# Optimization experiments

Measured on AMD Instinct MI355X. Metric: run time of the kernel, lower is better.

The kernel has to match this reference:

```python
import jax, jax.numpy as jnp
import numpy as np


def setup_inputs() -> dict:
    key = jax.random.key(0)
    ks = jax.random.split(key, 5)
    B, D, U = 16384, 512, 512
    return {
        "inputs": jax.random.normal(ks[0], (B, D), dtype=jnp.float32),
        "h_prev": jax.random.normal(ks[1], (B, U), dtype=jnp.float32),
        "update_kernel": jax.random.normal(ks[2], (D + U, U), dtype=jnp.float32) * 0.03,
        "reset_kernel": jax.random.normal(ks[3], (D + U, U), dtype=jnp.float32) * 0.03,
        "hidden_kernel": jax.random.normal(ks[4], (D + U, U), dtype=jnp.float32) * 0.03,
        "update_bias": jnp.zeros((U,), dtype=jnp.float32),
        "reset_bias": jnp.zeros((U,), dtype=jnp.float32),
        "hidden_bias": jnp.zeros((U,), dtype=jnp.float32),
    }


def reference(inputs, h_prev, update_kernel, reset_kernel, hidden_kernel,
              update_bias, reset_bias, hidden_bias):
    # fused_input: [B, D+U]
    fused = jnp.concatenate([inputs, h_prev], axis=-1)
    zg = jax.nn.sigmoid(fused @ update_kernel + update_bias)   # update gate [B,U]
    rg = jax.nn.sigmoid(fused @ reset_kernel + reset_bias)     # reset gate  [B,U]
    h_tilde = jnp.tanh(
        jnp.concatenate([inputs, rg * h_prev], axis=-1) @ hidden_kernel + hidden_bias
    )
    ht = (1.0 - zg) * h_prev + zg * h_tilde
    return ht
```

## Files before the change

### kernel.cpp

```cpp
#include <hip/hip_runtime.h>
#include <hip/hip_bf16.h>
#include <math.h>

typedef __attribute__((ext_vector_type(4))) float f32x4;
typedef __attribute__((ext_vector_type(8))) float f32x8;
typedef __bf16 bf16x8 __attribute__((ext_vector_type(8)));
typedef unsigned short u16;
typedef u16 u16x8 __attribute__((ext_vector_type(8)));
typedef void __attribute__((address_space(1))) * as1p;
typedef void __attribute__((address_space(3))) * as3p;

__device__ __forceinline__ unsigned short f2bf(float f) {
    union { float f; unsigned int u; } v; v.f = f;
    unsigned int u = v.u;
    u += 0x7fffu + ((u >> 16) & 1u);
    return (unsigned short)(u >> 16);
}

__device__ __forceinline__ float bf2f(unsigned short b) {
    union { unsigned int u; float f; } v;
    v.u = ((unsigned int)b) << 16;
    return v.f;
}

__device__ __forceinline__ float fast_tanh(float v) {
    float vc = fminf(fmaxf(v, -15.f), 15.f);
    float e = __expf(2.f * vc);
    return (e - 1.f) / (e + 1.f);
}

__global__ void prep_k(const float* __restrict__ x, const float* __restrict__ h,
                       const float* __restrict__ wz, const float* __restrict__ wrr,
                       const float* __restrict__ wh,
                       u16* __restrict__ xb, u16* __restrict__ hb,
                       u16* __restrict__ wzt, u16* __restrict__ wrt, u16* __restrict__ wht) {
    __shared__ float t[32][33];
    int bid = blockIdx.x;
    int tid = threadIdx.x;
    if (bid < 2048) {
        const int n4 = 16384 * 512 / 4;
        int i = bid * 256 + tid;
        const int stride = 2048 * 256;
        const float4* x4 = (const float4*)x;
        const float4* h4 = (const float4*)h;
        ushort4* xb4 = (ushort4*)xb;
        ushort4* hb4 = (ushort4*)hb;
        for (; i < n4; i += stride) {
            float4 v = x4[i];
            xb4[i] = make_ushort4(f2bf(v.x), f2bf(v.y), f2bf(v.z), f2bf(v.w));
            float4 w = h4[i];
            hb4[i] = make_ushort4(f2bf(w.x), f2bf(w.y), f2bf(w.z), f2bf(w.w));
        }
    } else {
        int b = bid - 2048;
        int z = b >> 9;
        int rem = b & 511;
        const float* src = (z == 0) ? wz : (z == 1) ? wrr : wh;
        u16* dst = (z == 0) ? wzt : (z == 1) ? wrt : wht;
        int n0 = (rem & 15) * 32;
        int k0 = (rem >> 4) * 32;
        int tx = tid & 31, ty = tid >> 5;
#pragma unroll
        for (int i = 0; i < 4; ++i)
            t[ty + i * 8][tx] = src[(size_t)(k0 + ty + i * 8) * 512 + n0 + tx];
        __syncthreads();
#pragma unroll
        for (int i = 0; i < 4; ++i)
            dst[(size_t)(n0 + ty + i * 8) * 1024 + k0 + tx] = f2bf(t[tx][ty + i * 8]);
    }
}

__device__ __forceinline__ void stage32(const u16* g, int gstride, u16* region, int tid) {
#pragma unroll
    for (int i = 0; i < 2; ++i) {
        int ob = i * 4096 + ((tid >> 6) << 10);
        int o = ob + ((tid & 63) << 4);
        int row = o >> 6;
        int cb = (o & 63) ^ ((row & 3) << 4);
        const u16* gp = g + (size_t)row * gstride + (cb >> 1);
        __builtin_amdgcn_global_load_lds((as1p)(void*)gp, (as3p)(void*)(region + (ob >> 1)), 16, 0, 0);
    }
}

__device__ __forceinline__ bf16x8 ld32(const u16* region, int r, int kb) {
    int byte = (r << 6) + (kb ^ ((r & 3) << 4));
    return *(const bf16x8*)((const char*)region + byte);
}

__device__ __forceinline__ void compute32(const u16* LA, const u16* LB,
                                          int wr, int wc, int l, f32x4 (&acc)[4][4]) {
    int fr = l & 15;
    int kbb = (l >> 4) << 4;
    bf16x8 a[4], b[4];
#pragma unroll
    for (int m = 0; m < 4; ++m)
        a[m] = ld32(LA, wr * 64 + m * 16 + fr, kbb);
#pragma unroll
    for (int n = 0; n < 4; ++n)
        b[n] = ld32(LB, wc * 64 + n * 16 + fr, kbb);
#pragma unroll
    for (int m = 0; m < 4; ++m)
#pragma unroll
        for (int n = 0; n < 4; ++n)
            acc[m][n] = __builtin_amdgcn_mfma_f32_16x16x32_bf16(a[m], b[n], acc[m][n], 0, 0, 0);
}

template<typename AF, typename BF>
__device__ __forceinline__ void kloop32(AF ga, BF gb, u16* lds, int tid,
                                        int wr, int wc, int l, f32x4 (&acc)[4][4]) {
    stage32(ga(0), 512, lds, tid);
    stage32(gb(0), 1024, lds + 4096, tid);
    __syncthreads();
#pragma unroll
    for (int i = 0; i < 31; ++i) {
        u16* nxt = lds + ((i + 1) & 1) * 8192;
        const u16* cur = lds + (i & 1) * 8192;
        stage32(ga(i + 1), 512, nxt, tid);
        stage32(gb(i + 1), 1024, nxt + 4096, tid);
        compute32(cur, cur + 4096, wr, wc, l, acc);
        __syncthreads();
    }
    compute32(lds + 8192, lds + 8192 + 4096, wr, wc, l, acc);
}

__device__ __forceinline__ void scatter_half(float* tf, const f32x4 (&acc)[4][4],
                                             int wc, int l) {
    int colb = wc * 64;
    int rowb = (l >> 4) << 2;
#pragma unroll
    for (int n = 0; n < 4; ++n) {
        int col = colb + n * 16 + (l & 15);
#pragma unroll
        for (int m = 0; m < 4; ++m) {
            int row0 = rowb + m * 16;
#pragma unroll
            for (int r = 0; r < 4; ++r)
                tf[(row0 + r) * 128 + col] = acc[m][n][r];
        }
    }
}

__global__ __launch_bounds__(256, 4) void gz_k(
    const u16* __restrict__ Xb, const u16* __restrict__ Hb, const u16* __restrict__ Wt,
    const float* __restrict__ ub, u16* __restrict__ zgb) {
    __shared__ u16 lds[2 * 8192];
    int tid = threadIdx.x;
    int l = tid & 63, w = tid >> 6;
    int wr = w >> 1, wc = w & 1;
    int swz = (blockIdx.x & 7) * 64 + (blockIdx.x >> 3);
    int mb = swz >> 2, nb = swz & 3;
    int m0 = mb * 128, n0 = nb * 128;
    f32x4 acc[4][4];
#pragma unroll
    for (int m = 0; m < 4; ++m)
#pragma unroll
        for (int n = 0; n < 4; ++n) acc[m][n] = (f32x4){0.f, 0.f, 0.f, 0.f};

    auto ga = [&](int t) -> const u16* {
        return (t < 16) ? (Xb + (size_t)m0 * 512 + t * 32)
                        : (Hb + (size_t)m0 * 512 + (t - 16) * 32);
    };
    auto gb = [&](int t) -> const u16* { return Wt + (size_t)n0 * 1024 + t * 32; };
    kloop32(ga, gb, lds, tid, wr, wc, l, acc);

    float* tf = (float*)lds;
#pragma unroll
    for (int half = 0; half < 2; ++half) {
        __syncthreads();
        if (wr == half) scatter_half(tf, acc, wc, l);
        __syncthreads();
#pragma unroll
        for (int it = 0; it < 4; ++it) {
            int chunk = it * 256 + tid;
            int row = chunk >> 4;
            int c8 = (chunk & 15) << 3;
            f32x8 v8 = *(const f32x8*)&tf[row * 128 + c8];
            int gcol = n0 + c8;
            f32x8 ubv = *(const f32x8*)&ub[gcol];
            u16x8 o;
#pragma unroll
            for (int j = 0; j < 8; ++j)
                o[j] = f2bf(1.f / (1.f + __expf(-(v8[j] + ubv[j]))));
            *(u16x8*)&zgb[(size_t)(m0 + half * 64 + row) * 512 + gcol] = o;
        }
    }
}

__global__ __launch_bounds__(256, 4) void gr_k(
    const u16* __restrict__ Xb, const u16* __restrict__ Hb, const u16* __restrict__ Wt,
    const float* __restrict__ rb_, u16* __restrict__ rgh) {
    __shared__ u16 lds[2 * 8192];
    int tid = threadIdx.x;
    int l = tid & 63, w = tid >> 6;
    int wr = w >> 1, wc = w & 1;
    int swz = (blockIdx.x & 7) * 64 + (blockIdx.x >> 3);
    int mb = swz >> 2, nb = swz & 3;
    int m0 = mb * 128, n0 = nb * 128;
    f32x4 acc[4][4];
#pragma unroll
    for (int m = 0; m < 4; ++m)
#pragma unroll
        for (int n = 0; n < 4; ++n) acc[m][n] = (f32x4){0.f, 0.f, 0.f, 0.f};

    auto ga = [&](int t) -> const u16* {
        return (t < 16) ? (Xb + (size_t)m0 * 512 + t * 32)
                        : (Hb + (size_t)m0 * 512 + (t - 16) * 32);
    };
    auto gb = [&](int t) -> const u16* { return Wt + (size_t)n0 * 1024 + t * 32; };
    kloop32(ga, gb, lds, tid, wr, wc, l, acc);

    float* tf = (float*)lds;
#pragma unroll
    for (int half = 0; half < 2; ++half) {
        __syncthreads();
        if (wr == half) scatter_half(tf, acc, wc, l);
        __syncthreads();
#pragma unroll
        for (int it = 0; it < 4; ++it) {
            int chunk = it * 256 + tid;
            int row = chunk >> 4;
            int c8 = (chunk & 15) << 3;
            f32x8 v8 = *(const f32x8*)&tf[row * 128 + c8];
            int gcol = n0 + c8;
            size_t gbase = (size_t)(m0 + half * 64 + row) * 512 + gcol;
            f32x8 rbv = *(const f32x8*)&rb_[gcol];
            u16x8 h8 = *(const u16x8*)&Hb[gbase];
            u16x8 o;
#pragma unroll
            for (int j = 0; j < 8; ++j) {
                float s = 1.f / (1.f + __expf(-(v8[j] + rbv[j])));
                o[j] = f2bf(s * bf2f(h8[j]));
            }
            *(u16x8*)&rgh[gbase] = o;
        }
    }
}

__global__ __launch_bounds__(256, 4) void gh_k(
    const u16* __restrict__ Xb, const u16* __restrict__ rgh, const u16* __restrict__ Wt,
    const float* __restrict__ hp, const u16* __restrict__ zgb, const float* __restrict__ hb,
    float* __restrict__ out) {
    __shared__ u16 lds[2 * 8192];
    int tid = threadIdx.x;
    int l = tid & 63, w = tid >> 6;
    int wr = w >> 1, wc = w & 1;
    int swz = (blockIdx.x & 7) * 64 + (blockIdx.x >> 3);
    int mb = swz >> 2, nb = swz & 3;
    int m0 = mb * 128, n0 = nb * 128;
    f32x4 acc[4][4];
#pragma unroll
    for (int m = 0; m < 4; ++m)
#pragma unroll
        for (int n = 0; n < 4; ++n) acc[m][n] = (f32x4){0.f, 0.f, 0.f, 0.f};

    auto ga = [&](int t) -> const u16* {
        return (t < 16) ? (Xb + (size_t)m0 * 512 + t * 32)
                        : (rgh + (size_t)m0 * 512 + (t - 16) * 32);
    };
    auto gb = [&](int t) -> const u16* { return Wt + (size_t)n0 * 1024 + t * 32; };
    kloop32(ga, gb, lds, tid, wr, wc, l, acc);

    float* tf = (float*)lds;
#pragma unroll
    for (int half = 0; half < 2; ++half) {
        __syncthreads();
        if (wr == half) scatter_half(tf, acc, wc, l);
        __syncthreads();
#pragma unroll
        for (int it = 0; it < 4; ++it) {
            int chunk = it * 256 + tid;
            int row = chunk >> 4;
            int c8 = (chunk & 15) << 3;
            f32x8 v8 = *(const f32x8*)&tf[row * 128 + c8];
            int gcol = n0 + c8;
            size_t gbase = (size_t)(m0 + half * 64 + row) * 512 + gcol;
            f32x8 hbv = *(const f32x8*)&hb[gcol];
            f32x8 h8 = *(const f32x8*)&hp[gbase];
            u16x8 z8 = *(const u16x8*)&zgb[gbase];
            f32x8 o;
#pragma unroll
            for (int j = 0; j < 8; ++j) {
                float t = fast_tanh(v8[j] + hbv[j]);
                float z = bf2f(z8[j]);
                o[j] = h8[j] + z * (t - h8[j]);
            }
            *(f32x8*)&out[gbase] = o;
        }
    }
}

extern "C" void kernel_launch(void* const* d_in, const int* in_sizes, int n_in,
                              void* d_out, int out_size, void* d_ws, size_t ws_size,
                              hipStream_t stream) {
    const float* x  = (const float*)d_in[0];
    const float* h  = (const float*)d_in[1];
    const float* wz = (const float*)d_in[2];
    const float* wr = (const float*)d_in[3];
    const float* wh = (const float*)d_in[4];
    const float* ub = (const float*)d_in[5];
    const float* rb = (const float*)d_in[6];
    const float* hb = (const float*)d_in[7];
    float* out = (float*)d_out;

    const int B = 16384;
    char* ws = (char*)d_ws;
    size_t off = 0;
    u16* Xb  = (u16*)(ws + off); off += (size_t)B * 512 * 2;
    u16* Hb  = (u16*)(ws + off); off += (size_t)B * 512 * 2;
    u16* Wzt = (u16*)(ws + off); off += (size_t)512 * 1024 * 2;
    u16* Wrt = (u16*)(ws + off); off += (size_t)512 * 1024 * 2;
    u16* Wht = (u16*)(ws + off); off += (size_t)512 * 1024 * 2;
    u16* rgh = (u16*)(ws + off); off += (size_t)B * 512 * 2;
    u16* zgb = (u16*)(ws + off); off += (size_t)B * 512 * 2;

    prep_k<<<2048 + 1536, 256, 0, stream>>>(x, h, wz, wr, wh, Xb, Hb, Wzt, Wrt, Wht);

    gz_k<<<512, 256, 0, stream>>>(Xb, Hb, Wzt, ub, zgb);
    gr_k<<<512, 256, 0, stream>>>(Xb, Hb, Wrt, rb, rgh);
    gh_k<<<512, 256, 0, stream>>>(Xb, rgh, Wht, h, zgb, hb, out);
}
```

Baseline: 98.77 us.

## Merge z and r gate GEMMs and use a 4-deep LDS ring pipeline

Replaces the double-buffered K loop with a 4-slot LDS ring that prefetches three stages ahead. Waits use explicit vmcnt counts plus raw barriers instead of __syncthreads. The separate update-gate and reset-gate kernels become one 1024-block launch that picks the weight and epilogue per N tile, removing a launch and letting the shared X/H tiles be reused across both gates. LDS per block grows to 64KB and launch bounds drop to 2 blocks per CU, which lowers occupancy. Correctness depends on the hand-counted vmcnt values matching the number of loads each stage32 issues.

```diff
diff --git a/kernel.cpp b/kernel.cpp
--- a/kernel.cpp
+++ b/kernel.cpp
@@ -9,6 +9,12 @@
 typedef u16 u16x8 __attribute__((ext_vector_type(8)));
 typedef void __attribute__((address_space(1))) * as1p;
 typedef void __attribute__((address_space(3))) * as3p;
+
+#define WAITVM8() asm volatile("s_waitcnt vmcnt(8)" ::: "memory")
+#define WAITVM4() asm volatile("s_waitcnt vmcnt(4)" ::: "memory")
+#define WAITVM0() asm volatile("s_waitcnt vmcnt(0)" ::: "memory")
+#define SBAR()    __builtin_amdgcn_s_barrier()
+#define SCHEDB()  __builtin_amdgcn_sched_barrier(0)
 
 __device__ __forceinline__ unsigned short f2bf(float f) {
     union { float f; unsigned int u; } v; v.f = f;
@@ -106,21 +112,30 @@
 }
 
 template<typename AF, typename BF>
-__device__ __forceinline__ void kloop32(AF ga, BF gb, u16* lds, int tid,
-                                        int wr, int wc, int l, f32x4 (&acc)[4][4]) {
-    stage32(ga(0), 512, lds, tid);
-    stage32(gb(0), 1024, lds + 4096, tid);
-    __syncthreads();
-#pragma unroll
-    for (int i = 0; i < 31; ++i) {
-        u16* nxt = lds + ((i + 1) & 1) * 8192;
-        const u16* cur = lds + (i & 1) * 8192;
-        stage32(ga(i + 1), 512, nxt, tid);
-        stage32(gb(i + 1), 1024, nxt + 4096, tid);
+__device__ __forceinline__ void kring(AF ga, BF gb, u16* lds, int tid,
+                                      int wr, int wc, int l, f32x4 (&acc)[4][4]) {
+#pragma unroll
+    for (int t = 0; t < 3; ++t) {
+        u16* b = lds + t * 8192;
+        stage32(ga(t), 512, b, tid);
+        stage32(gb(t), 1024, b + 4096, tid);
+    }
+#pragma unroll
+    for (int i = 0; i < 29; ++i) {
+        WAITVM8(); SCHEDB();
+        SBAR(); SCHEDB();
+        u16* nb_ = lds + ((i + 3) & 3) * 8192;
+        stage32(ga(i + 3), 512, nb_, tid);
+        stage32(gb(i + 3), 1024, nb_ + 4096, tid);
+        const u16* cur = lds + (i & 3) * 8192;
         compute32(cur, cur + 4096, wr, wc, l, acc);
-        __syncthreads();
-    }
-    compute32(lds + 8192, lds + 8192 + 4096, wr, wc, l, acc);
+    }
+    WAITVM8(); SCHEDB(); SBAR(); SCHEDB();
+    { const u16* cur = lds + (29 & 3) * 8192; compute32(cur, cur + 4096, wr, wc, l, acc); }
+    WAITVM4(); SCHEDB(); SBAR(); SCHEDB();
+    { const u16* cur = lds + (30 & 3) * 8192; compute32(cur, cur + 4096, wr, wc, l, acc); }
+    WAITVM0(); SCHEDB(); SBAR(); SCHEDB();
+    { const u16* cur = lds + (31 & 3) * 8192; compute32(cur, cur + 4096, wr, wc, l, acc); }
 }
 
 __device__ __forceinline__ void scatter_half(float* tf, const f32x4 (&acc)[4][4],
@@ -140,10 +155,76 @@
     }
 }
 
-__global__ __launch_bounds__(256, 4) void gz_k(
-    const u16* __restrict__ Xb, const u16* __restrict__ Hb, const u16* __restrict__ Wt,
-    const float* __restrict__ ub, u16* __restrict__ zgb) {
-    __shared__ u16 lds[2 * 8192];
+__global__ __launch_bounds__(256, 2) void zr_k(
+    const u16* __restrict__ Xb, const u16* __restrict__ Hb,
+    const u16* __restrict__ Wzt, const u16* __restrict__ Wrt,
+    const float* __restrict__ ub, const float* __restrict__ rb_,
+    u16* __restrict__ zgb, u16* __restrict__ rgh) {
+    __shared__ u16 lds[4 * 8192];
+    int tid = threadIdx.x;
+    int l = tid & 63, w = tid >> 6;
+    int wr = w >> 1, wc = w & 1;
+    int swz = (blockIdx.x & 7) * 128 + (blockIdx.x >> 3);
+    int mb = swz >> 3, nb = swz & 7;
+    int m0 = mb * 128, n0 = nb * 128;
+    bool isZ = (n0 < 512);
+    const u16* Wt = isZ ? Wzt : Wrt;
+    int nw = isZ ? n0 : (n0 - 512);
+
+    f32x4 acc[4][4];
+#pragma unroll
+    for (int m = 0; m < 4; ++m)
+#pragma unroll
+        for (int n = 0; n < 4; ++n) acc[m][n] = (f32x4){0.f, 0.f, 0.f, 0.f};
+
+    auto ga = [&](int t) -> const u16* {
+        return (t < 16) ? (Xb + (size_t)m0 * 512 + t * 32)
+                        : (Hb + (size_t)m0 * 512 + (t - 16) * 32);
+    };
+    auto gb = [&](int t) -> const u16* { return Wt + (size_t)nw * 1024 + t * 32; };
+    kring(ga, gb, lds, tid, wr, wc, l, acc);
+
+    float* tf = (float*)lds;
+#pragma unroll
+    for (int half = 0; half < 2; ++half) {
+        __syncthreads();
+        if (wr == half) scatter_half(tf, acc, wc, l);
+        __syncthreads();
+#pragma unroll
+        for (int it = 0; it < 4; ++it) {
+            int chunk = it * 256 + tid;
+            int row = chunk >> 4;
+            int c8 = (chunk & 15) << 3;
+            f32x8 v8 = *(const f32x8*)&tf[row * 128 + c8];
+            int gcol = nw + c8;
+            size_t gbase = (size_t)(m0 + half * 64 + row) * 512 + gcol;
+            if (isZ) {
+                f32x8 bv = *(const f32x8*)&ub[gcol];
+                u16x8 o;
+#pragma unroll
+                for (int j = 0; j < 8; ++j)
+                    o[j] = f2bf(1.f / (1.f + __expf(-(v8[j] + bv[j]))));
+                *(u16x8*)&zgb[gbase] = o;
+            } else {
+                f32x8 bv = *(const f32x8*)&rb_[gcol];
+                u16x8 h8 = *(const u16x8*)&Hb[gbase];
+                u16x8 o;
+#pragma unroll
+                for (int j = 0; j < 8; ++j) {
+                    float s = 1.f / (1.f + __expf(-(v8[j] + bv[j])));
+                    o[j] = f2bf(s * bf2f(h8[j]));
+                }
+                *(u16x8*)&rgh[gbase] = o;
+            }
+        }
+    }
+}
+
+__global__ __launch_bounds__(256, 2) void gh_k(
+    const u16* __restrict__ Xb, const u16* __restrict__ rgh, const u16* __restrict__ Wt,
+    const float* __restrict__ hp, const u16* __restrict__ zgb, const float* __restrict__ hb,
+    float* __restrict__ out) {
+    __shared__ u16 lds[4 * 8192];
     int tid = threadIdx.x;
     int l = tid & 63, w = tid >> 6;
     int wr = w >> 1, wc = w & 1;
@@ -158,107 +239,10 @@
 
     auto ga = [&](int t) -> const u16* {
         return (t < 16) ? (Xb + (size_t)m0 * 512 + t * 32)
-                        : (Hb + (size_t)m0 * 512 + (t - 16) * 32);
-    };
-    auto gb = [&](int t) -> const u16* { return Wt + (size_t)n0 * 1024 + t * 32; };
-    kloop32(ga, gb, lds, tid, wr, wc, l, acc);
-
-    float* tf = (float*)lds;
-#pragma unroll
-    for (int half = 0; half < 2; ++half) {
-        __syncthreads();
-        if (wr == half) scatter_half(tf, acc, wc, l);
-        __syncthreads();
-#pragma unroll
-        for (int it = 0; it < 4; ++it) {
-            int chunk = it * 256 + tid;
-            int row = chunk >> 4;
-            int c8 = (chunk & 15) << 3;
-            f32x8 v8 = *(const f32x8*)&tf[row * 128 + c8];
-            int gcol = n0 + c8;
-            f32x8 ubv = *(const f32x8*)&ub[gcol];
-            u16x8 o;
-#pragma unroll
-            for (int j = 0; j < 8; ++j)
-                o[j] = f2bf(1.f / (1.f + __expf(-(v8[j] + ubv[j]))));
-            *(u16x8*)&zgb[(size_t)(m0 + half * 64 + row) * 512 + gcol] = o;
-        }
-    }
-}
-
-__global__ __launch_bounds__(256, 4) void gr_k(
-    const u16* __restrict__ Xb, const u16* __restrict__ Hb, const u16* __restrict__ Wt,
-    const float* __restrict__ rb_, u16* __restrict__ rgh) {
-    __shared__ u16 lds[2 * 8192];
-    int tid = threadIdx.x;
-    int l = tid & 63, w = tid >> 6;
-    int wr = w >> 1, wc = w & 1;
-    int swz = (blockIdx.x & 7) * 64 + (blockIdx.x >> 3);
-    int mb = swz >> 2, nb = swz & 3;
-    int m0 = mb * 128, n0 = nb * 128;
-    f32x4 acc[4][4];
-#pragma unroll
-    for (int m = 0; m < 4; ++m)
-#pragma unroll
-        for (int n = 0; n < 4; ++n) acc[m][n] = (f32x4){0.f, 0.f, 0.f, 0.f};
-
-    auto ga = [&](int t) -> const u16* {
-        return (t < 16) ? (Xb + (size_t)m0 * 512 + t * 32)
-                        : (Hb + (size_t)m0 * 512 + (t - 16) * 32);
-    };
-    auto gb = [&](int t) -> const u16* { return Wt + (size_t)n0 * 1024 + t * 32; };
-    kloop32(ga, gb, lds, tid, wr, wc, l, acc);
-
-    float* tf = (float*)lds;
-#pragma unroll
-    for (int half = 0; half < 2; ++half) {
-        __syncthreads();
-        if (wr == half) scatter_half(tf, acc, wc, l);
-        __syncthreads();
-#pragma unroll
-        for (int it = 0; it < 4; ++it) {
-            int chunk = it * 256 + tid;
-            int row = chunk >> 4;
-            int c8 = (chunk & 15) << 3;
-            f32x8 v8 = *(const f32x8*)&tf[row * 128 + c8];
-            int gcol = n0 + c8;
-            size_t gbase = (size_t)(m0 + half * 64 + row) * 512 + gcol;
-            f32x8 rbv = *(const f32x8*)&rb_[gcol];
-            u16x8 h8 = *(const u16x8*)&Hb[gbase];
-            u16x8 o;
-#pragma unroll
-            for (int j = 0; j < 8; ++j) {
-                float s = 1.f / (1.f + __expf(-(v8[j] + rbv[j])));
-                o[j] = f2bf(s * bf2f(h8[j]));
-            }
-            *(u16x8*)&rgh[gbase] = o;
-        }
-    }
-}
-
-__global__ __launch_bounds__(256, 4) void gh_k(
-    const u16* __restrict__ Xb, const u16* __restrict__ rgh, const u16* __restrict__ Wt,
-    const float* __restrict__ hp, const u16* __restrict__ zgb, const float* __restrict__ hb,
-    float* __restrict__ out) {
-    __shared__ u16 lds[2 * 8192];
-    int tid = threadIdx.x;
-    int l = tid & 63, w = tid >> 6;
-    int wr = w >> 1, wc = w & 1;
-    int swz = (blockIdx.x & 7) * 64 + (blockIdx.x >> 3);
-    int mb = swz >> 2, nb = swz & 3;
-    int m0 = mb * 128, n0 = nb * 128;
-    f32x4 acc[4][4];
-#pragma unroll
-    for (int m = 0; m < 4; ++m)
-#pragma unroll
-        for (int n = 0; n < 4; ++n) acc[m][n] = (f32x4){0.f, 0.f, 0.f, 0.f};
-
-    auto ga = [&](int t) -> const u16* {
-        return (t < 16) ? (Xb + (size_t)m0 * 512 + t * 32)
                         : (rgh + (size_t)m0 * 512 + (t - 16) * 32);
     };
     auto gb = [&](int t) -> const u16* { return Wt + (size_t)n0 * 1024 + t * 32; };
-    kloop32(ga, gb, lds, tid, wr, wc, l, acc);
+    kring(ga, gb, lds, tid, wr, wc, l, acc);
 
     float* tf = (float*)lds;
 #pragma unroll
@@ -315,7 +299,6 @@
 
     prep_k<<<2048 + 1536, 256, 0, stream>>>(x, h, wz, wr, wh, Xb, Hb, Wzt, Wrt, Wht);
 
-    gz_k<<<512, 256, 0, stream>>>(Xb, Hb, Wzt, ub, zgb);
-    gr_k<<<512, 256, 0, stream>>>(Xb, Hb, Wrt, rb, rgh);
+    zr_k<<<1024, 256, 0, stream>>>(Xb, Hb, Wzt, Wrt, ub, rb, zgb, rgh);
     gh_k<<<512, 256, 0, stream>>>(Xb, rgh, Wht, h, zgb, hb, out);
 }
```

After: 98.66 us. About the same (-0.1%).
